# Kernel optimization log

Measured on AMD Instinct MI355X. Metric: run time of the kernel, lower is better.

## Reference

```python
import jax, jax.numpy as jnp
import numpy as np

N = 100000   # nodes
E = 800000   # edges
IN = 128     # input features
HID = 128    # hidden channels (= trans out_channels, heads=1)
OUT = 64     # output classes
EPS = 1e-5
ALPHA = 0.5


def _lin(k, fi, fo):
    kw, kb = jax.random.split(k)
    w = jax.random.normal(kw, (fi, fo), jnp.float32) / np.float32(np.sqrt(fi))
    b = jax.random.normal(kb, (fo,), jnp.float32) * 0.01
    return w, b


def setup_inputs() -> dict:
    key = jax.random.key(0)
    k = jax.random.split(key, 12)
    x = jax.random.normal(k[0], (N, IN), jnp.float32)
    edge_index = jax.random.randint(k[1], (2, E), 0, N)
    edge_type = jax.random.randint(k[2], (E,), 0, 2)
    edge_weight = jax.random.uniform(k[3], (E,), jnp.float32)
    t_fc_w, t_fc_b = _lin(k[4], IN, HID)
    wq, wq_b = _lin(k[5], HID, HID)
    wk, wk_b = _lin(k[6], HID, HID)
    wv, wv_b = _lin(k[7], HID, HID)
    g_fc_w, g_fc_b = _lin(k[8], IN, HID)
    g_w1, g_b1 = _lin(k[9], HID, HID)
    g_w2, g_b2 = _lin(k[10], HID, HID)
    out_w, out_b = _lin(k[11], 2 * HID, OUT)
    ones = jnp.ones((HID,), jnp.float32)
    zeros = jnp.zeros((HID,), jnp.float32)
    return dict(
        x=x, edge_weight=edge_weight,
        t_fc_w=t_fc_w, t_fc_b=t_fc_b, t_ln0_g=ones, t_ln0_b=zeros,
        wq=wq, wq_b=wq_b, wk=wk, wk_b=wk_b, wv=wv, wv_b=wv_b,
        t_ln1_g=ones, t_ln1_b=zeros,
        g_fc_w=g_fc_w, g_fc_b=g_fc_b,
        bn0_g=ones, bn0_b=zeros, bn0_m=zeros, bn0_v=ones,
        g_w1=g_w1, g_b1=g_b1, bn1_g=ones, bn1_b=zeros, bn1_m=zeros, bn1_v=ones,
        g_w2=g_w2, g_b2=g_b2, bn2_g=ones, bn2_b=zeros, bn2_m=zeros, bn2_v=ones,
        out_w=out_w, out_b=out_b,
        edge_index=edge_index, edge_type=edge_type,
    )


def _ln(x, g, b):
    m = x.mean(-1, keepdims=True)
    v = ((x - m) ** 2).mean(-1, keepdims=True)
    return (x - m) / jnp.sqrt(v + EPS) * g + b


def _bn(x, g, b, m, v):  # eval-mode BatchNorm1d (running stats)
    return (x - m) / jnp.sqrt(v + EPS) * g + b


def _full_attn(q, k, v):
    # q:[N,H,M] k:[L,H,M] v:[L,H,D]; global (Frobenius) norm as in torch.norm(qs, p=2)
    q = q / jnp.linalg.norm(q)
    k = k / jnp.linalg.norm(k)
    n = q.shape[0]
    kvs = jnp.einsum('lhm,lhd->hmd', k, v)
    num = jnp.einsum('nhm,hmd->nhd', q, kvs) + n * v
    ksum = k.sum(0)  # [H,M]
    denom = jnp.einsum('nhm,hm->nh', q, ksum)[..., None] + n
    return num / denom


def _hetero(x, row, col, ew, mask, W, b):
    # degree over edges of this type, normalized SpMM: out[col] += val * x[row]
    d = jax.ops.segment_sum(mask.astype(jnp.float32), col, num_segments=N)
    val = ew / jnp.sqrt(d[col] * d[row])
    val = jnp.where(mask, jnp.nan_to_num(val, nan=0.0, posinf=0.0, neginf=0.0), 0.0)
    agg = jax.ops.segment_sum(val[:, None] * x[row], col, num_segments=N)
    return agg @ W + b


def reference(x, edge_weight, t_fc_w, t_fc_b, t_ln0_g, t_ln0_b, wq, wq_b, wk, wk_b,
              wv, wv_b, t_ln1_g, t_ln1_b, g_fc_w, g_fc_b, bn0_g, bn0_b, bn0_m, bn0_v,
              g_w1, g_b1, bn1_g, bn1_b, bn1_m, bn1_v, g_w2, g_b2, bn2_g, bn2_b, bn2_m,
              bn2_v, out_w, out_b, edge_index, edge_type):
    relu = jax.nn.relu
    # --- transformer (kernelized global attention) branch ---
    h = relu(_ln(x @ t_fc_w + t_fc_b, t_ln0_g, t_ln0_b))
    q = (h @ wq + wq_b)[:, None, :]   # [N,1,HID]
    kk = (h @ wk + wk_b)[:, None, :]
    vv = (h @ wv + wv_b)[:, None, :]
    z = _full_attn(q, kk, vv).mean(axis=1)
    x_trans = relu(_ln(ALPHA * z + (1.0 - ALPHA) * h, t_ln1_g, t_ln1_b))
    # --- alternating hetero GNN branch ---
    row, col = edge_index[0], edge_index[1]
    g = relu(_bn(x @ g_fc_w + g_fc_b, bn0_g, bn0_b, bn0_m, bn0_v))
    g1 = relu(_bn(_hetero(g, row, col, edge_weight, edge_type == 0, g_w1, g_b1),
                  bn1_g, bn1_b, bn1_m, bn1_v)) + g
    g2 = relu(_bn(_hetero(g1, row, col, edge_weight, edge_type == 1, g_w2, g_b2),
                  bn2_g, bn2_b, bn2_m, bn2_v)) + g1
    return jnp.tanh(jnp.concatenate([x_trans, g2], axis=1) @ out_w + out_b)
```

## Files before the change

### kernel.cpp

```cpp
#include <hip/hip_runtime.h>
#include <cmath>

#define EPSF 1e-5f

typedef __bf16 bfx8 __attribute__((ext_vector_type(8)));
typedef float  f32x4 __attribute__((ext_vector_type(4)));

__device__ __forceinline__ float4 ld4(const float* p){ return *(const float4*)p; }
__device__ __forceinline__ unsigned f2bf(float f){
    unsigned u = __builtin_bit_cast(unsigned, f);
    return (u + 0x7FFFu + ((u >> 16) & 1u)) >> 16;
}
__device__ __forceinline__ float bf2f(unsigned u){
    return __builtin_bit_cast(float, u << 16);
}
__device__ __forceinline__ bfx8 mfma_ld(const char* p){ return *(const bfx8*)p; }

__global__ __launch_bounds__(256)
void wconv_all(const float* __restrict__ s0, const float* __restrict__ s1,
               const float* __restrict__ s2, const float* __restrict__ s3,
               const float* __restrict__ s4, const float* __restrict__ s5,
               unsigned short* __restrict__ WT)
{
    int seg = blockIdx.x >> 6;
    int i = (blockIdx.x & 63)*256 + threadIdx.x;
    if (seg < 5) {
        const float* s = seg==0?s0: seg==1?s1: seg==2?s2: seg==3?s3: s4;
        int c = i >> 7, k = i & 127;
        WT[seg*16384 + i] = (unsigned short)f2bf(s[(size_t)k*128 + c]);
    } else {
        int c = i >> 8, k = i & 255;
        WT[5*16384 + i] = (unsigned short)f2bf(s5[(size_t)k*64 + c]);
    }
}

__global__ __launch_bounds__(256)
void fused_front(const float* __restrict__ x,
                 const unsigned short* __restrict__ wt_tfc,
                 const unsigned short* __restrict__ wt_wv,
                 const unsigned short* __restrict__ wt_gfc,
                 const float* __restrict__ tfcb, const float* __restrict__ ln0g,
                 const float* __restrict__ ln0b, const float* __restrict__ wvb,
                 const float* __restrict__ ln1g, const float* __restrict__ ln1b,
                 const float* __restrict__ gfcb, const float* __restrict__ bn0g,
                 const float* __restrict__ bn0b, const float* __restrict__ bn0m,
                 const float* __restrict__ bn0v,
                 unsigned short* __restrict__ XTb, float* __restrict__ Gf,
                 unsigned short* __restrict__ Gb, int nrows)
{
    __shared__ __align__(16) char lds[65536];
    char*  Xr  = lds;
    char*  Hr  = lds + 16384;
    char*  Wr  = lds + 32768;
    float* Cst = (float*)Wr;
    const int tid  = threadIdx.x;
    const int row0 = blockIdx.x * 64;
    const int w  = tid >> 6, ln = tid & 63, lr = ln & 15, lg = ln >> 4;
    const int ksw = (lr & 7) << 4;

    #pragma unroll
    for (int i = 0; i < 4; ++i) {
        int c  = tid + i*256, r = c >> 4, k0 = (c & 15)*8;
        uint4 v4 = make_uint4(0,0,0,0);
        if (row0 + r < nrows) {
            float4 f0 = ld4(&x[(size_t)(row0+r)*128 + k0]);
            float4 f1 = ld4(&x[(size_t)(row0+r)*128 + k0 + 4]);
            v4.x = f2bf(f0.x) | (f2bf(f0.y) << 16);
            v4.y = f2bf(f0.z) | (f2bf(f0.w) << 16);
            v4.z = f2bf(f1.x) | (f2bf(f1.y) << 16);
            v4.w = f2bf(f1.z) | (f2bf(f1.w) << 16);
        }
        *(uint4*)&Xr[r*256 + ((k0*2) ^ ((r&7)<<4))] = v4;
    }
    #pragma unroll
    for (int i = 0; i < 8; ++i) {
        int c = tid + i*256, wr2 = c >> 4, k0 = (c & 15)*8;
        *(uint4*)&Wr[wr2*256 + ((k0*2) ^ ((wr2&7)<<4))] =
            *(const uint4*)&wt_tfc[(size_t)wr2*128 + k0];
    }
    __syncthreads();

    f32x4 acc[8];
    #pragma unroll
    for (int nf = 0; nf < 8; ++nf) acc[nf] = (f32x4){0.f,0.f,0.f,0.f};

    const char* Ab = &Xr[(w*16 + lr)*256];
    #pragma unroll
    for (int ks = 0; ks < 4; ++ks) {
        int kb = (ks*32 + lg*8)*2;
        bfx8 a = mfma_ld(Ab + (kb ^ ksw));
        #pragma unroll
        for (int nf = 0; nf < 8; ++nf) {
            bfx8 b = mfma_ld(&Wr[(nf*16 + lr)*256] + (kb ^ ksw));
            acc[nf] = __builtin_amdgcn_mfma_f32_16x16x32_bf16(a, b, acc[nf], 0, 0, 0);
        }
    }
    float h[8][4];
    {
        float gl[8], bl[8];
        #pragma unroll
        for (int nf = 0; nf < 8; ++nf) {
            int c = nf*16 + lr;
            gl[nf] = ln0g[c]; bl[nf] = ln0b[c];
            float bb = tfcb[c];
            #pragma unroll
            for (int i = 0; i < 4; ++i) h[nf][i] = acc[nf][i] + bb;
        }
        #pragma unroll
        for (int i = 0; i < 4; ++i) {
            float s = 0.f, s2 = 0.f;
            #pragma unroll
            for (int nf = 0; nf < 8; ++nf) { s += h[nf][i]; s2 += h[nf][i]*h[nf][i]; }
            #pragma unroll
            for (int m = 1; m < 16; m <<= 1) { s += __shfl_xor(s, m); s2 += __shfl_xor(s2, m); }
            float mean = s * (1.f/128.f);
            float inv  = rsqrtf(s2 * (1.f/128.f) - mean*mean + EPSF);
            #pragma unroll
            for (int nf = 0; nf < 8; ++nf)
                h[nf][i] = fmaxf((h[nf][i]-mean)*inv*gl[nf] + bl[nf], 0.f);
        }
    }
    __syncthreads();
    #pragma unroll
    for (int nf = 0; nf < 8; ++nf)
        #pragma unroll
        for (int i = 0; i < 4; ++i) {
            int r = w*16 + lg*4 + i;
            Cst[r*128 + ((nf*16 + lr) ^ ((r&7)<<2))] = h[nf][i];
        }
    __syncthreads();
    #pragma unroll
    for (int i = 0; i < 8; ++i) {
        int c = tid + i*256, r = c >> 5, k4 = (c & 31)*4;
        f32x4 v = *(f32x4*)&Cst[r*128 + (k4 ^ ((r&7)<<2))];
        uint2 pk;
        pk.x = f2bf(v[0]) | (f2bf(v[1]) << 16);
        pk.y = f2bf(v[2]) | (f2bf(v[3]) << 16);
        *(uint2*)&Hr[r*256 + ((k4*2) ^ ((r&7)<<4))] = pk;
    }
    __syncthreads();
    #pragma unroll
    for (int i = 0; i < 8; ++i) {
        int c = tid + i*256, wr2 = c >> 4, k0 = (c & 15)*8;
        *(uint4*)&Wr[wr2*256 + ((k0*2) ^ ((wr2&7)<<4))] =
            *(const uint4*)&wt_wv[(size_t)wr2*128 + k0];
    }
    __syncthreads();
    #pragma unroll
    for (int nf = 0; nf < 8; ++nf) acc[nf] = (f32x4){0.f,0.f,0.f,0.f};
    const char* Hb = &Hr[(w*16 + lr)*256];
    #pragma unroll
    for (int ks = 0; ks < 4; ++ks) {
        int kb = (ks*32 + lg*8)*2;
        bfx8 a = mfma_ld(Hb + (kb ^ ksw));
        #pragma unroll
        for (int nf = 0; nf < 8; ++nf) {
            bfx8 b = mfma_ld(&Wr[(nf*16 + lr)*256] + (kb ^ ksw));
            acc[nf] = __builtin_amdgcn_mfma_f32_16x16x32_bf16(a, b, acc[nf], 0, 0, 0);
        }
    }
    {
        float gl[8], bl[8];
        #pragma unroll
        for (int nf = 0; nf < 8; ++nf) {
            int c = nf*16 + lr;
            gl[nf] = ln1g[c]; bl[nf] = ln1b[c];
            float bb = wvb[c];
            #pragma unroll
            for (int i = 0; i < 4; ++i)
                h[nf][i] = 0.5f*(acc[nf][i] + bb) + 0.5f*h[nf][i];
        }
        #pragma unroll
        for (int i = 0; i < 4; ++i) {
            float s = 0.f, s2 = 0.f;
            #pragma unroll
            for (int nf = 0; nf < 8; ++nf) { s += h[nf][i]; s2 += h[nf][i]*h[nf][i]; }
            #pragma unroll
            for (int m = 1; m < 16; m <<= 1) { s += __shfl_xor(s, m); s2 += __shfl_xor(s2, m); }
            float mean = s * (1.f/128.f);
            float inv  = rsqrtf(s2 * (1.f/128.f) - mean*mean + EPSF);
            #pragma unroll
            for (int nf = 0; nf < 8; ++nf)
                h[nf][i] = fmaxf((h[nf][i]-mean)*inv*gl[nf] + bl[nf], 0.f);
        }
    }
    __syncthreads();
    #pragma unroll
    for (int nf = 0; nf < 8; ++nf)
        #pragma unroll
        for (int i = 0; i < 4; ++i) {
            int r = w*16 + lg*4 + i;
            Cst[r*128 + ((nf*16 + lr) ^ ((r&7)<<2))] = h[nf][i];
        }
    __syncthreads();
    #pragma unroll
    for (int i = 0; i < 8; ++i) {
        int c = tid + i*256, r = c >> 5, k4 = (c & 31)*4;
        if (row0 + r < nrows) {
            f32x4 v = *(f32x4*)&Cst[r*128 + (k4 ^ ((r&7)<<2))];
            uint2 pk;
            pk.x = f2bf(v[0]) | (f2bf(v[1]) << 16);
            pk.y = f2bf(v[2]) | (f2bf(v[3]) << 16);
            *(uint2*)&XTb[(size_t)(row0+r)*128 + k4] = pk;
        }
    }
    __syncthreads();
    #pragma unroll
    for (int i = 0; i < 8; ++i) {
        int c = tid + i*256, wr2 = c >> 4, k0 = (c & 15)*8;
        *(uint4*)&Wr[wr2*256 + ((k0*2) ^ ((wr2&7)<<4))] =
            *(const uint4*)&wt_gfc[(size_t)wr2*128 + k0];
    }
    __syncthreads();
    #pragma unroll
    for (int nf = 0; nf < 8; ++nf) acc[nf] = (f32x4){0.f,0.f,0.f,0.f};
    #pragma unroll
    for (int ks = 0; ks < 4; ++ks) {
        int kb = (ks*32 + lg*8)*2;
        bfx8 a = mfma_ld(Ab + (kb ^ ksw));
        #pragma unroll
        for (int nf = 0; nf < 8; ++nf) {
            bfx8 b = mfma_ld(&Wr[(nf*16 + lr)*256] + (kb ^ ksw));
            acc[nf] = __builtin_amdgcn_mfma_f32_16x16x32_bf16(a, b, acc[nf], 0, 0, 0);
        }
    }
    #pragma unroll
    for (int nf = 0; nf < 8; ++nf) {
        int c = nf*16 + lr;
        float sc = bn0g[c] * rsqrtf(bn0v[c] + EPSF);
        float sh = bn0b[c] - bn0m[c]*sc;
        float bb = gfcb[c];
        #pragma unroll
        for (int i = 0; i < 4; ++i)
            h[nf][i] = fmaxf((acc[nf][i] + bb)*sc + sh, 0.f);
    }
    __syncthreads();
    #pragma unroll
    for (int nf = 0; nf < 8; ++nf)
        #pragma unroll
        for (int i = 0; i < 4; ++i) {
            int r = w*16 + lg*4 + i;
            Cst[r*128 + ((nf*16 + lr) ^ ((r&7)<<2))] = h[nf][i];
        }
    __syncthreads();
    #pragma unroll
    for (int i = 0; i < 8; ++i) {
        int c = tid + i*256, r = c >> 5, k4 = (c & 31)*4;
        if (row0 + r < nrows) {
            f32x4 v = *(f32x4*)&Cst[r*128 + (k4 ^ ((r&7)<<2))];
            *(f32x4*)&Gf[(size_t)(row0+r)*128 + k4] = v;
            uint2 pk;
            pk.x = f2bf(v[0]) | (f2bf(v[1]) << 16);
            pk.y = f2bf(v[2]) | (f2bf(v[3]) << 16);
            *(uint2*)&Gb[(size_t)(row0+r)*128 + k4] = pk;
        }
    }
}

template<int EPI, bool ABF16, bool OUTF32, bool OUTBF16>
__global__ __launch_bounds__(256)
void mgemm(const void* __restrict__ Aptr, const unsigned short* __restrict__ WT,
           const float* __restrict__ bias, float* __restrict__ Cf,
           unsigned short* __restrict__ Cb, int nrows,
           const float* __restrict__ p0, const float* __restrict__ p1,
           const float* __restrict__ p2, const float* __restrict__ p3,
           const float* __restrict__ resid)
{
    __shared__ __align__(16) char lds[49152];
    const int tid  = threadIdx.x;
    const int row0 = blockIdx.x * 64;

    #pragma unroll
    for (int i = 0; i < 4; ++i) {
        int c  = tid + i*256;
        int r  = c >> 4;
        int k0 = (c & 15) * 8;
        uint4 w = make_uint4(0,0,0,0);
        if (row0 + r < nrows) {
            if constexpr (ABF16) {
                w = *(const uint4*)((const unsigned short*)Aptr + (size_t)(row0+r)*128 + k0);
            } else {
                const float* A = (const float*)Aptr;
                float4 f0 = ld4(A + (size_t)(row0+r)*128 + k0);
                float4 f1 = ld4(A + (size_t)(row0+r)*128 + k0 + 4);
                w.x = f2bf(f0.x) | (f2bf(f0.y) << 16);
                w.y = f2bf(f0.z) | (f2bf(f0.w) << 16);
                w.z = f2bf(f1.x) | (f2bf(f1.y) << 16);
                w.w = f2bf(f1.z) | (f2bf(f1.w) << 16);
            }
        }
        *(uint4*)&lds[r*256 + ((k0*2) ^ ((r&7)<<4))] = w;
    }
    #pragma unroll
    for (int i = 0; i < 8; ++i) {
        int c  = tid + i*256;
        int wr = c >> 4;
        int k0 = (c & 15) * 8;
        *(uint4*)&lds[16384 + wr*256 + ((k0*2) ^ ((wr&7)<<4))] =
            *(const uint4*)&WT[(size_t)wr*128 + k0];
    }
    __syncthreads();

    const int w  = tid >> 6;
    const int ln = tid & 63;
    const int lr = ln & 15;
    const int lg = ln >> 4;
    const int ksw = (lr & 7) << 4;

    f32x4 acc[8];
    #pragma unroll
    for (int nf = 0; nf < 8; ++nf) acc[nf] = (f32x4){0.f,0.f,0.f,0.f};

    const char* Abase = &lds[(w*16 + lr) * 256];
    #pragma unroll
    for (int ks = 0; ks < 4; ++ks) {
        int kb = (ks*32 + lg*8) * 2;
        bfx8 a = *(const bfx8*)(Abase + (kb ^ ksw));
        #pragma unroll
        for (int nf = 0; nf < 8; ++nf) {
            bfx8 b = *(const bfx8*)(&lds[16384 + (nf*16 + lr)*256] + (kb ^ ksw));
            acc[nf] = __builtin_amdgcn_mfma_f32_16x16x32_bf16(a, b, acc[nf], 0, 0, 0);
        }
    }

    float t[8][4];
    #pragma unroll
    for (int nf = 0; nf < 8; ++nf) {
        float bb = bias[nf*16 + lr];
        #pragma unroll
        for (int i = 0; i < 4; ++i) t[nf][i] = acc[nf][i] + bb;
    }
    if constexpr (EPI >= 2) {
        #pragma unroll
        for (int nf = 0; nf < 8; ++nf) {
            int c = nf*16 + lr;
            float sc = p0[c] * rsqrtf(p3[c] + EPSF);
            float sh = p1[c] - p2[c]*sc;
            #pragma unroll
            for (int i = 0; i < 4; ++i) t[nf][i] = fmaxf(t[nf][i]*sc + sh, 0.f);
        }
    }

    __syncthreads();
    float* Cst = (float*)lds;
    #pragma unroll
    for (int nf = 0; nf < 8; ++nf)
        #pragma unroll
        for (int i = 0; i < 4; ++i)
            Cst[(w*16 + lg*4 + i)*132 + nf*16 + lr] = t[nf][i];
    __syncthreads();
    #pragma unroll
    for (int i = 0; i < 8; ++i) {
        int c  = tid + i*256;
        int r  = c >> 5;
        int c4 = (c & 31) * 4;
        if (row0 + r >= nrows) continue;
        f32x4 v = *(f32x4*)&Cst[r*132 + c4];
        if constexpr (EPI == 3) {
            float4 rr = ld4(resid + (size_t)(row0+r)*128 + c4);
            v.x += rr.x; v.y += rr.y; v.z += rr.z; v.w += rr.w;
        }
        if constexpr (OUTF32)
            *(f32x4*)&Cf[(size_t)(row0+r)*128 + c4] = v;
        if constexpr (OUTBF16) {
            uint2 pk;
            pk.x = f2bf(v.x) | (f2bf(v.y) << 16);
            pk.y = f2bf(v.z) | (f2bf(v.w) << 16);
            *(uint2*)&Cb[(size_t)(row0+r)*128 + c4] = pk;
        }
    }
}

__global__ __launch_bounds__(256)
void out_mfma(const unsigned short* __restrict__ XTb,
              const unsigned short* __restrict__ G2b,
              const unsigned short* __restrict__ WT,
              const float* __restrict__ B, float* __restrict__ out, int nrows)
{
    __shared__ __align__(16) char lds[65536];
    const int tid  = threadIdx.x;
    const int row0 = blockIdx.x * 64;

    #pragma unroll
    for (int i = 0; i < 8; ++i) {
        int c  = tid + i*256;
        int r  = c >> 5;
        int k0 = (c & 31) * 8;
        uint4 w = make_uint4(0,0,0,0);
        if (row0 + r < nrows) {
            const unsigned short* src = (k0 < 128)
                ? &XTb[(size_t)(row0+r)*128 + k0]
                : &G2b[(size_t)(row0+r)*128 + (k0-128)];
            w = *(const uint4*)src;
        }
        *(uint4*)&lds[r*512 + ((k0*2) ^ ((r&7)<<4))] = w;
    }
    #pragma unroll
    for (int i = 0; i < 8; ++i) {
        int c  = tid + i*256;
        int wr = c >> 5;
        int k0 = (c & 31) * 8;
        *(uint4*)&lds[32768 + wr*512 + ((k0*2) ^ ((wr&7)<<4))] =
            *(const uint4*)&WT[(size_t)wr*256 + k0];
    }
    __syncthreads();

    const int w  = tid >> 6;
    const int ln = tid & 63;
    const int lr = ln & 15;
    const int lg = ln >> 4;
    const int ksw = (lr & 7) << 4;

    f32x4 acc[4];
    #pragma unroll
    for (int nf = 0; nf < 4; ++nf) acc[nf] = (f32x4){0.f,0.f,0.f,0.f};

    const char* Abase = &lds[(w*16 + lr) * 512];
    #pragma unroll
    for (int ks = 0; ks < 8; ++ks) {
        int kb = (ks*32 + lg*8) * 2;
        bfx8 a = *(const bfx8*)(Abase + (kb ^ ksw));
        #pragma unroll
        for (int nf = 0; nf < 4; ++nf) {
            bfx8 b = *(const bfx8*)(&lds[32768 + (nf*16 + lr)*512] + (kb ^ ksw));
            acc[nf] = __builtin_amdgcn_mfma_f32_16x16x32_bf16(a, b, acc[nf], 0, 0, 0);
        }
    }
    #pragma unroll
    for (int nf = 0; nf < 4; ++nf) {
        float bb = B[nf*16 + lr];
        #pragma unroll
        for (int i = 0; i < 4; ++i) {
            int r = row0 + w*16 + lg*4 + i;
            if (r < nrows)
                out[(size_t)r*64 + nf*16 + lr] = tanhf(acc[nf][i] + bb);
        }
    }
}

__global__ __launch_bounds__(256)
void edge_hist(const int* __restrict__ col, const int* __restrict__ et,
               int* __restrict__ cnt, int n, int ne)
{
    int e = blockIdx.x*256 + threadIdx.x;
    if (e >= ne) return;
    atomicAdd(&cnt[et[e]*n + col[e]], 1);
}

__global__ __launch_bounds__(1024)
void scan_block(const int* __restrict__ cnt, int* __restrict__ off,
                int* __restrict__ bsum, int n)
{
    __shared__ int s[1024];
    const int t = threadIdx.x;
    const int i = blockIdx.x*1024 + t;
    int v = (i < n) ? cnt[i] : 0;
    s[t] = v;
    __syncthreads();
    #pragma unroll
    for (int d = 1; d < 1024; d <<= 1) {
        int u = (t >= d) ? s[t-d] : 0;
        __syncthreads();
        s[t] += u;
        __syncthreads();
    }
    if (i < n) off[i] = s[t] - v;
    if (t == 1023) bsum[blockIdx.x] = s[1023];
}

__global__ __launch_bounds__(256)
void scan_bsums(int* __restrict__ bsum, int nb)
{
    __shared__ int s[256];
    const int t = threadIdx.x;
    int v = (t < nb) ? bsum[t] : 0;
    s[t] = v;
    __syncthreads();
    #pragma unroll
    for (int d = 1; d < 256; d <<= 1) {
        int u = (t >= d) ? s[t-d] : 0;
        __syncthreads();
        s[t] += u;
        __syncthreads();
    }
    if (t < nb) bsum[t] = s[t] - v;
}

__global__ __launch_bounds__(1024)
void scan_add(int* __restrict__ off, const int* __restrict__ bsum, int n)
{
    int i = blockIdx.x*1024 + threadIdx.x;
    if (i < n) off[i] += bsum[blockIdx.x];
}

__global__ __launch_bounds__(256)
void edge_fill(const int* __restrict__ row_idx, const int* __restrict__ col_idx,
               const int* __restrict__ et, const float* __restrict__ ew,
               const int* __restrict__ cnt, const int* __restrict__ off,
               int* __restrict__ cursor, uint2* __restrict__ ePack, int n, int ne)
{
    int e = blockIdx.x*256 + threadIdx.x;
    if (e >= ne) return;
    int t = et[e], c = col_idx[e], r = row_idx[e];
    int ic = t*n + c;
    int pos = atomicAdd(&cursor[ic], 1);
    int idx = off[ic] + pos;
    int p = cnt[ic] * cnt[t*n + r];
    float val = (p > 0) ? ew[e] * rsqrtf((float)p) : 0.f;
    ePack[idx] = make_uint2((unsigned)r, __builtin_bit_cast(unsigned, val));
}

__global__ __launch_bounds__(256)
void hetero_gather(const unsigned short* __restrict__ Gb,
                   const uint2* __restrict__ ePack,
                   const int* __restrict__ cnt, const int* __restrict__ off,
                   unsigned short* __restrict__ AGGb, int n)
{
    int node = blockIdx.x*4 + (threadIdx.x >> 6);
    if (node >= n) return;
    const int lane = threadIdx.x & 63;
    const int base = off[node];
    const int m = cnt[node];
    float ax = 0.f, ay = 0.f;
    int i = 0;
    for (; i + 1 < m; i += 2) {
        uint2 p0 = ePack[base+i];
        uint2 p1 = ePack[base+i+1];
        unsigned g0 = *(const unsigned*)&Gb[(size_t)p0.x*128 + lane*2];
        unsigned g1 = *(const unsigned*)&Gb[(size_t)p1.x*128 + lane*2];
        float v0 = __builtin_bit_cast(float, p0.y);
        float v1 = __builtin_bit_cast(float, p1.y);
        ax += v0*bf2f(g0 & 0xffff) + v1*bf2f(g1 & 0xffff);
        ay += v0*bf2f(g0 >> 16)    + v1*bf2f(g1 >> 16);
    }
    if (i < m) {
        uint2 p0 = ePack[base+i];
        unsigned g0 = *(const unsigned*)&Gb[(size_t)p0.x*128 + lane*2];
        float v0 = __builtin_bit_cast(float, p0.y);
        ax += v0*bf2f(g0 & 0xffff);
        ay += v0*bf2f(g0 >> 16);
    }
    unsigned pk = f2bf(ax) | (f2bf(ay) << 16);
    *(unsigned*)&AGGb[(size_t)node*128 + lane*2] = pk;
}

extern "C" void kernel_launch(void* const* d_in, const int* in_sizes, int n_in,
                              void* d_out, int out_size, void* d_ws, size_t ws_size,
                              hipStream_t stream)
{
    const float* x      = (const float*)d_in[0];
    const float* ew     = (const float*)d_in[1];
    const float* t_fc_w = (const float*)d_in[2];
    const float* t_fc_b = (const float*)d_in[3];
    const float* ln0g   = (const float*)d_in[4];
    const float* ln0b   = (const float*)d_in[5];
    const float* wvw    = (const float*)d_in[10];
    const float* wvb    = (const float*)d_in[11];
    const float* ln1g   = (const float*)d_in[12];
    const float* ln1b   = (const float*)d_in[13];
    const float* gfcw   = (const float*)d_in[14];
    const float* gfcb   = (const float*)d_in[15];
    const float* bn0g   = (const float*)d_in[16];
    const float* bn0b   = (const float*)d_in[17];
    const float* bn0m   = (const float*)d_in[18];
    const float* bn0v   = (const float*)d_in[19];
    const float* gw1    = (const float*)d_in[20];
    const float* gb1    = (const float*)d_in[21];
    const float* bn1g   = (const float*)d_in[22];
    const float* bn1b   = (const float*)d_in[23];
    const float* bn1m   = (const float*)d_in[24];
    const float* bn1v   = (const float*)d_in[25];
    const float* gw2    = (const float*)d_in[26];
    const float* gb2    = (const float*)d_in[27];
    const float* bn2g   = (const float*)d_in[28];
    const float* bn2b   = (const float*)d_in[29];
    const float* bn2m   = (const float*)d_in[30];
    const float* bn2v   = (const float*)d_in[31];
    const float* outw   = (const float*)d_in[32];
    const float* outb   = (const float*)d_in[33];
    const int*   ei     = (const int*)d_in[34];
    const int*   et     = (const int*)d_in[35];

    const int N = 100000, E = 800000;
    const size_t NF = (size_t)N*128;
    float* F1 = (float*)d_ws;
    float* F2 = F1 + NF;
    unsigned short* B1 = (unsigned short*)(F2 + NF);
    unsigned short* B2 = B1 + NF;
    unsigned short* B3 = B2 + NF;
    unsigned short* B4 = B3 + NF;
    unsigned short* WT = B4 + NF;
    unsigned short* wt_tfc = WT;
    unsigned short* wt_wv  = WT + 16384;
    unsigned short* wt_gfc = WT + 2*16384;
    unsigned short* wt_g1  = WT + 3*16384;
    unsigned short* wt_g2  = WT + 4*16384;
    unsigned short* wt_out = WT + 5*16384;
    int*   cnt    = (int*)(WT + 6*16384);
    int*   cursor = cnt + 2*N;
    int*   off    = cursor + 2*N;
    uint2* ePack  = (uint2*)(off + 2*N);
    int*   bsum   = (int*)(ePack + E);

    dim3 blk(256);
    const int nb64 = (N + 63) / 64;
    const int* row_idx = ei;
    const int* col_idx = ei + E;
    const int nscan = 2*N;
    const int nsb = (nscan + 1023) / 1024;

    hipMemsetAsync(cnt, 0, 4*(size_t)N*sizeof(int), stream);
    edge_hist<<<(E + 255)/256, blk, 0, stream>>>(col_idx, et, cnt, N, E);
    scan_block<<<nsb, 1024, 0, stream>>>(cnt, off, bsum, nscan);
    scan_bsums<<<1, 256, 0, stream>>>(bsum, nsb);
    scan_add<<<nsb, 1024, 0, stream>>>(off, bsum, nscan);
    edge_fill<<<(E + 255)/256, blk, 0, stream>>>(row_idx, col_idx, et, ew,
                                                 cnt, off, cursor, ePack, N, E);

    wconv_all<<<384, blk, 0, stream>>>(t_fc_w, wvw, gfcw, gw1, gw2, outw, WT);

    fused_front<<<nb64, blk, 0, stream>>>(x, wt_tfc, wt_wv, wt_gfc,
        t_fc_b, ln0g, ln0b, wvb, ln1g, ln1b,
        gfcb, bn0g, bn0b, bn0m, bn0v, B4, F2, B3, N);

    hetero_gather<<<(N + 3)/4, blk, 0, stream>>>(B3, ePack, cnt,     off,     B1, N);
    mgemm<3,true,true,true><<<nb64, blk, 0, stream>>>(B1, wt_g1, gb1, F1, B3, N,
                                                      bn1g, bn1b, bn1m, bn1v, F2);
    hetero_gather<<<(N + 3)/4, blk, 0, stream>>>(B3, ePack, cnt + N, off + N, B1, N);
    mgemm<3,true,false,true><<<nb64, blk, 0, stream>>>(B1, wt_g2, gb2, nullptr, B2, N,
                                                       bn2g, bn2b, bn2m, bn2v, F1);

    out_mfma<<<nb64, blk, 0, stream>>>(B4, B2, wt_out, outb, (float*)d_out, N);
}
```

Before: 321.0 us.

## Shrink LDS footprint in fused_front and out_mfma to raise occupancy

fused_front is reordered so the GNN branch (x@g_fc_w + BN) runs right after the first LN, letting the x tile buffer be reused for the bf16 h tile. The separate H buffer goes away and LDS drops from 64KB to about 49KB, with a padded stride-132 staging layout in place of the XOR swizzle. out_mfma splits its K=256 reduction into two 128-wide halves that reuse a 32KB LDS area instead of 64KB. The aim is more resident blocks per CU, at the cost of extra barriers and serialized loads in out_mfma, and possibly more register pressure from keeping h live across the GNN GEMM.

```diff
diff --git a/kernel.cpp b/kernel.cpp
--- a/kernel.cpp
+++ b/kernel.cpp
@@ -48,10 +48,9 @@
                  unsigned short* __restrict__ XTb, float* __restrict__ Gf,
                  unsigned short* __restrict__ Gb, int nrows)
 {
-    __shared__ __align__(16) char lds[65536];
-    char*  Xr  = lds;
-    char*  Hr  = lds + 16384;
-    char*  Wr  = lds + 32768;
+    __shared__ __align__(16) char lds[50176];
+    char*  Ar  = lds;
+    char*  Wr  = lds + 16384;
     float* Cst = (float*)Wr;
     const int tid  = threadIdx.x;
     const int row0 = blockIdx.x * 64;
@@ -70,7 +69,7 @@
             v4.z = f2bf(f1.x) | (f2bf(f1.y) << 16);
             v4.w = f2bf(f1.z) | (f2bf(f1.w) << 16);
         }
-        *(uint4*)&Xr[r*256 + ((k0*2) ^ ((r&7)<<4))] = v4;
+        *(uint4*)&Ar[r*256 + ((k0*2) ^ ((r&7)<<4))] = v4;
     }
     #pragma unroll
     for (int i = 0; i < 8; ++i) {
@@ -84,7 +83,7 @@
     #pragma unroll
     for (int nf = 0; nf < 8; ++nf) acc[nf] = (f32x4){0.f,0.f,0.f,0.f};
 
-    const char* Ab = &Xr[(w*16 + lr)*256];
+    const char* Ab = &Ar[(w*16 + lr)*256];
     #pragma unroll
     for (int ks = 0; ks < 4; ++ks) {
         int kb = (ks*32 + lg*8)*2;
@@ -118,90 +117,6 @@
             #pragma unroll
             for (int nf = 0; nf < 8; ++nf)
                 h[nf][i] = fmaxf((h[nf][i]-mean)*inv*gl[nf] + bl[nf], 0.f);
-        }
-    }
-    __syncthreads();
-    #pragma unroll
-    for (int nf = 0; nf < 8; ++nf)
-        #pragma unroll
-        for (int i = 0; i < 4; ++i) {
-            int r = w*16 + lg*4 + i;
-            Cst[r*128 + ((nf*16 + lr) ^ ((r&7)<<2))] = h[nf][i];
-        }
-    __syncthreads();
-    #pragma unroll
-    for (int i = 0; i < 8; ++i) {
-        int c = tid + i*256, r = c >> 5, k4 = (c & 31)*4;
-        f32x4 v = *(f32x4*)&Cst[r*128 + (k4 ^ ((r&7)<<2))];
-        uint2 pk;
-        pk.x = f2bf(v[0]) | (f2bf(v[1]) << 16);
-        pk.y = f2bf(v[2]) | (f2bf(v[3]) << 16);
-        *(uint2*)&Hr[r*256 + ((k4*2) ^ ((r&7)<<4))] = pk;
-    }
-    __syncthreads();
-    #pragma unroll
-    for (int i = 0; i < 8; ++i) {
-        int c = tid + i*256, wr2 = c >> 4, k0 = (c & 15)*8;
-        *(uint4*)&Wr[wr2*256 + ((k0*2) ^ ((wr2&7)<<4))] =
-            *(const uint4*)&wt_wv[(size_t)wr2*128 + k0];
-    }
-    __syncthreads();
-    #pragma unroll
-    for (int nf = 0; nf < 8; ++nf) acc[nf] = (f32x4){0.f,0.f,0.f,0.f};
-    const char* Hb = &Hr[(w*16 + lr)*256];
-    #pragma unroll
-    for (int ks = 0; ks < 4; ++ks) {
-        int kb = (ks*32 + lg*8)*2;
-        bfx8 a = mfma_ld(Hb + (kb ^ ksw));
-        #pragma unroll
-        for (int nf = 0; nf < 8; ++nf) {
-            bfx8 b = mfma_ld(&Wr[(nf*16 + lr)*256] + (kb ^ ksw));
-            acc[nf] = __builtin_amdgcn_mfma_f32_16x16x32_bf16(a, b, acc[nf], 0, 0, 0);
-        }
-    }
-    {
-        float gl[8], bl[8];
-        #pragma unroll
-        for (int nf = 0; nf < 8; ++nf) {
-            int c = nf*16 + lr;
-            gl[nf] = ln1g[c]; bl[nf] = ln1b[c];
-            float bb = wvb[c];
-            #pragma unroll
-            for (int i = 0; i < 4; ++i)
-                h[nf][i] = 0.5f*(acc[nf][i] + bb) + 0.5f*h[nf][i];
-        }
-        #pragma unroll
-        for (int i = 0; i < 4; ++i) {
-            float s = 0.f, s2 = 0.f;
-            #pragma unroll
-            for (int nf = 0; nf < 8; ++nf) { s += h[nf][i]; s2 += h[nf][i]*h[nf][i]; }
-            #pragma unroll
-            for (int m = 1; m < 16; m <<= 1) { s += __shfl_xor(s, m); s2 += __shfl_xor(s2, m); }
-            float mean = s * (1.f/128.f);
-            float inv  = rsqrtf(s2 * (1.f/128.f) - mean*mean + EPSF);
-            #pragma unroll
-            for (int nf = 0; nf < 8; ++nf)
-                h[nf][i] = fmaxf((h[nf][i]-mean)*inv*gl[nf] + bl[nf], 0.f);
-        }
-    }
-    __syncthreads();
-    #pragma unroll
-    for (int nf = 0; nf < 8; ++nf)
-        #pragma unroll
-        for (int i = 0; i < 4; ++i) {
-            int r = w*16 + lg*4 + i;
-            Cst[r*128 + ((nf*16 + lr) ^ ((r&7)<<2))] = h[nf][i];
-        }
-    __syncthreads();
-    #pragma unroll
-    for (int i = 0; i < 8; ++i) {
-        int c = tid + i*256, r = c >> 5, k4 = (c & 31)*4;
-        if (row0 + r < nrows) {
-            f32x4 v = *(f32x4*)&Cst[r*128 + (k4 ^ ((r&7)<<2))];
-            uint2 pk;
-            pk.x = f2bf(v[0]) | (f2bf(v[1]) << 16);
-            pk.y = f2bf(v[2]) | (f2bf(v[3]) << 16);
-            *(uint2*)&XTb[(size_t)(row0+r)*128 + k4] = pk;
         }
     }
     __syncthreads();
@@ -232,27 +147,104 @@
         float bb = gfcb[c];
         #pragma unroll
         for (int i = 0; i < 4; ++i)
-            h[nf][i] = fmaxf((acc[nf][i] + bb)*sc + sh, 0.f);
+            acc[nf][i] = fmaxf((acc[nf][i] + bb)*sc + sh, 0.f);
     }
     __syncthreads();
     #pragma unroll
     for (int nf = 0; nf < 8; ++nf)
         #pragma unroll
-        for (int i = 0; i < 4; ++i) {
-            int r = w*16 + lg*4 + i;
-            Cst[r*128 + ((nf*16 + lr) ^ ((r&7)<<2))] = h[nf][i];
-        }
+        for (int i = 0; i < 4; ++i)
+            Cst[(w*16 + lg*4 + i)*132 + nf*16 + lr] = acc[nf][i];
     __syncthreads();
     #pragma unroll
     for (int i = 0; i < 8; ++i) {
         int c = tid + i*256, r = c >> 5, k4 = (c & 31)*4;
         if (row0 + r < nrows) {
-            f32x4 v = *(f32x4*)&Cst[r*128 + (k4 ^ ((r&7)<<2))];
+            f32x4 v = *(f32x4*)&Cst[r*132 + k4];
             *(f32x4*)&Gf[(size_t)(row0+r)*128 + k4] = v;
             uint2 pk;
             pk.x = f2bf(v[0]) | (f2bf(v[1]) << 16);
             pk.y = f2bf(v[2]) | (f2bf(v[3]) << 16);
             *(uint2*)&Gb[(size_t)(row0+r)*128 + k4] = pk;
+        }
+    }
+    __syncthreads();
+    #pragma unroll
+    for (int nf = 0; nf < 8; ++nf)
+        #pragma unroll
+        for (int i = 0; i < 4; ++i)
+            Cst[(w*16 + lg*4 + i)*132 + nf*16 + lr] = h[nf][i];
+    __syncthreads();
+    #pragma unroll
+    for (int i = 0; i < 8; ++i) {
+        int c = tid + i*256, r = c >> 5, k4 = (c & 31)*4;
+        f32x4 v = *(f32x4*)&Cst[r*132 + k4];
+        uint2 pk;
+        pk.x = f2bf(v[0]) | (f2bf(v[1]) << 16);
+        pk.y = f2bf(v[2]) | (f2bf(v[3]) << 16);
+        *(uint2*)&Ar[r*256 + ((k4*2) ^ ((r&7)<<4))] = pk;
+    }
+    __syncthreads();
+    #pragma unroll
+    for (int i = 0; i < 8; ++i) {
+        int c = tid + i*256, wr2 = c >> 4, k0 = (c & 15)*8;
+        *(uint4*)&Wr[wr2*256 + ((k0*2) ^ ((wr2&7)<<4))] =
+            *(const uint4*)&wt_wv[(size_t)wr2*128 + k0];
+    }
+    __syncthreads();
+    #pragma unroll
+    for (int nf = 0; nf < 8; ++nf) acc[nf] = (f32x4){0.f,0.f,0.f,0.f};
+    #pragma unroll
+    for (int ks = 0; ks < 4; ++ks) {
+        int kb = (ks*32 + lg*8)*2;
+        bfx8 a = mfma_ld(Ab + (kb ^ ksw));
+        #pragma unroll
+        for (int nf = 0; nf < 8; ++nf) {
+            bfx8 b = mfma_ld(&Wr[(nf*16 + lr)*256] + (kb ^ ksw));
+            acc[nf] = __builtin_amdgcn_mfma_f32_16x16x32_bf16(a, b, acc[nf], 0, 0, 0);
+        }
+    }
+    {
+        float gl[8], bl[8];
+        #pragma unroll
+        for (int nf = 0; nf < 8; ++nf) {
+            int c = nf*16 + lr;
+            gl[nf] = ln1g[c]; bl[nf] = ln1b[c];
+            float bb = wvb[c];
+            #pragma unroll
+            for (int i = 0; i < 4; ++i)
+                h[nf][i] = 0.5f*(acc[nf][i] + bb) + 0.5f*h[nf][i];
+        }
+        #pragma unroll
+        for (int i = 0; i < 4; ++i) {
+            float s = 0.f, s2 = 0.f;
+            #pragma unroll
+            for (int nf = 0; nf < 8; ++nf) { s += h[nf][i]; s2 += h[nf][i]*h[nf][i]; }
+            #pragma unroll
+            for (int m = 1; m < 16; m <<= 1) { s += __shfl_xor(s, m); s2 += __shfl_xor(s2, m); }
+            float mean = s * (1.f/128.f);
+            float inv  = rsqrtf(s2 * (1.f/128.f) - mean*mean + EPSF);
+            #pragma unroll
+            for (int nf = 0; nf < 8; ++nf)
+                h[nf][i] = fmaxf((h[nf][i]-mean)*inv*gl[nf] + bl[nf], 0.f);
+        }
+    }
+    __syncthreads();
+    #pragma unroll
+    for (int nf = 0; nf < 8; ++nf)
+        #pragma unroll
+        for (int i = 0; i < 4; ++i)
+            Cst[(w*16 + lg*4 + i)*132 + nf*16 + lr] = h[nf][i];
+    __syncthreads();
+    #pragma unroll
+    for (int i = 0; i < 8; ++i) {
+        int c = tid + i*256, r = c >> 5, k4 = (c & 31)*4;
+        if (row0 + r < nrows) {
+            f32x4 v = *(f32x4*)&Cst[r*132 + k4];
+            uint2 pk;
+            pk.x = f2bf(v[0]) | (f2bf(v[1]) << 16);
+            pk.y = f2bf(v[2]) | (f2bf(v[3]) << 16);
+            *(uint2*)&XTb[(size_t)(row0+r)*128 + k4] = pk;
         }
     }
 }
@@ -377,34 +369,11 @@
               const unsigned short* __restrict__ WT,
               const float* __restrict__ B, float* __restrict__ out, int nrows)
 {
-    __shared__ __align__(16) char lds[65536];
+    __shared__ __align__(16) char lds[32768];
+    char* Ar = lds;
+    char* Wr = lds + 16384;
     const int tid  = threadIdx.x;
     const int row0 = blockIdx.x * 64;
-
-    #pragma unroll
-    for (int i = 0; i < 8; ++i) {
-        int c  = tid + i*256;
-        int r  = c >> 5;
-        int k0 = (c & 31) * 8;
-        uint4 w = make_uint4(0,0,0,0);
-        if (row0 + r < nrows) {
-            const unsigned short* src = (k0 < 128)
-                ? &XTb[(size_t)(row0+r)*128 + k0]
-                : &G2b[(size_t)(row0+r)*128 + (k0-128)];
-            w = *(const uint4*)src;
-        }
-        *(uint4*)&lds[r*512 + ((k0*2) ^ ((r&7)<<4))] = w;
-    }
-    #pragma unroll
-    for (int i = 0; i < 8; ++i) {
-        int c  = tid + i*256;
-        int wr = c >> 5;
-        int k0 = (c & 31) * 8;
-        *(uint4*)&lds[32768 + wr*512 + ((k0*2) ^ ((wr&7)<<4))] =
-            *(const uint4*)&WT[(size_t)wr*256 + k0];
-    }
-    __syncthreads();
-
     const int w  = tid >> 6;
     const int ln = tid & 63;
     const int lr = ln & 15;
@@ -415,15 +384,34 @@
     #pragma unroll
     for (int nf = 0; nf < 4; ++nf) acc[nf] = (f32x4){0.f,0.f,0.f,0.f};
 
-    const char* Abase = &lds[(w*16 + lr) * 512];
-    #pragma unroll
-    for (int ks = 0; ks < 8; ++ks) {
-        int kb = (ks*32 + lg*8) * 2;
-        bfx8 a = *(const bfx8*)(Abase + (kb ^ ksw));
-        #pragma unroll
-        for (int nf = 0; nf < 4; ++nf) {
-            bfx8 b = *(const bfx8*)(&lds[32768 + (nf*16 + lr)*512] + (kb ^ ksw));
-            acc[nf] = __builtin_amdgcn_mfma_f32_16x16x32_bf16(a, b, acc[nf], 0, 0, 0);
+    #pragma unroll
+    for (int half = 0; half < 2; ++half) {
+        const unsigned short* Asrc = half ? G2b : XTb;
+        if (half) __syncthreads();
+        #pragma unroll
+        for (int i = 0; i < 4; ++i) {
+            int c  = tid + i*256, r = c >> 4, k0 = (c & 15)*8;
+            uint4 v = make_uint4(0,0,0,0);
+            if (row0 + r < nrows) v = *(const uint4*)&Asrc[(size_t)(row0+r)*128 + k0];
+            *(uint4*)&Ar[r*256 + ((k0*2) ^ ((r&7)<<4))] = v;
+        }
+        #pragma unroll
+        for (int i = 0; i < 4; ++i) {
+            int c  = tid + i*256, wr2 = c >> 4, k0 = (c & 15)*8;
+            *(uint4*)&Wr[wr2*256 + ((k0*2) ^ ((wr2&7)<<4))] =
+                *(const uint4*)&WT[(size_t)wr2*256 + half*128 + k0];
+        }
+        __syncthreads();
+        const char* Ab = &Ar[(w*16 + lr)*256];
+        #pragma unroll
+        for (int ks = 0; ks < 4; ++ks) {
+            int kb = (ks*32 + lg*8)*2;
+            bfx8 a = mfma_ld(Ab + (kb ^ ksw));
+            #pragma unroll
+            for (int nf = 0; nf < 4; ++nf) {
+                bfx8 b = mfma_ld(&Wr[(nf*16 + lr)*256] + (kb ^ ksw));
+                acc[nf] = __builtin_amdgcn_mfma_f32_16x16x32_bf16(a, b, acc[nf], 0, 0, 0);
+            }
         }
     }
     #pragma unroll
```

Measured after the change: 307.4 us. -4.2%, faster.
